# Optimization experiments

Measured on AMD Instinct MI355X. Metric: run time of the kernel, lower is better.

The kernel has to match this reference:

```python
import jax, jax.numpy as jnp
import numpy as np

N = 20000        # total nodes
E = 240000       # directed edges (avg in-degree 12); self-loops appended in reference
G = 50           # graphs in the batch
NPG = N // G     # nodes per graph
TD = 768         # text embedding dim
HC = 64          # hidden_channels
H = 8            # attention heads for conv1..conv3 (conv4 uses 1 head)
FD = 3 * HC * H + HC  # JK cat dim for num_layers=4
NEG = 0.2        # GATv2 leaky_relu negative slope
EPS = 1e-5       # GraphNorm eps


def setup_inputs() -> dict:
    key = jax.random.key(0)
    ks = iter(jax.random.split(key, 64))

    def w(shape, s=0.05):
        return jax.random.normal(next(ks), shape, dtype=jnp.float32) * s

    z = lambda *s: jnp.zeros(s, jnp.float32)
    o = lambda *s: jnp.ones(s, jnp.float32)

    inp = {
        'x': w((N, TD), 1.0),
        'edge_index': jax.random.randint(next(ks), (2, E), 0, N, dtype=jnp.int32),
        'batch': jnp.arange(N, dtype=jnp.int32) // NPG,
        'ptr': jnp.arange(G + 1, dtype=jnp.int32) * NPG,
        'tp_w': w((TD, HC)), 'tp_b': z(HC),
        'lin_w': w((FD, 1), 0.005), 'lin_b': z(1),
    }
    # GATv2Conv params: lin_l (source), lin_r (target), att, output bias
    for name, ind, heads, concat in [('c1', HC, H, True), ('c2', HC * H, H, True),
                                     ('c3', HC * H, H, True), ('c4', HC * H, 1, False)]:
        inp[name + '_wl'] = w((ind, heads * HC)); inp[name + '_bl'] = z(heads * HC)
        inp[name + '_wr'] = w((ind, heads * HC)); inp[name + '_br'] = z(heads * HC)
        inp[name + '_att'] = w((heads, HC))
        inp[name + '_bias'] = z(heads * HC if concat else HC)
    # GraphNorm params: weight, bias, mean_scale
    for name, d in [('n1', HC * H), ('n2', HC * H), ('n3', HC * H), ('n4', HC)]:
        inp[name + '_w'] = o(d); inp[name + '_b'] = z(d); inp[name + '_ms'] = o(d)
    return inp


def _gatv2(x, src, dst, wl, bl, wr, br, att, bias, heads, concat):
    # GATv2: e_ij = att . leaky_relu(W_l x_j + W_r x_i); alpha = softmax over in-neighbors of i
    xl = (x @ wl + bl).reshape(N, heads, HC)
    xr = (x @ wr + br).reshape(N, heads, HC)
    e = jax.nn.leaky_relu(xl[src] + xr[dst], NEG)           # [E', H, C]
    logit = jnp.einsum('ehc,hc->eh', e, att)                # [E', H]
    m = jax.ops.segment_max(logit, dst, num_segments=N)     # stable scatter-softmax
    p = jnp.exp(logit - m[dst])
    alpha = p / jax.ops.segment_sum(p, dst, num_segments=N)[dst]
    out = jax.ops.segment_sum(xl[src] * alpha[..., None], dst, num_segments=N)
    out = out.reshape(N, heads * HC) if concat else out.mean(axis=1)
    return out + bias


def _gnorm(x, batch, w, b, ms):
    # PyG GraphNorm: per-graph mean (scaled by mean_scale), per-graph std
    cnt = jax.ops.segment_sum(jnp.ones((N,), x.dtype), batch, num_segments=G)[:, None]
    mean = jax.ops.segment_sum(x, batch, num_segments=G) / cnt
    cen = x - ms * mean[batch]
    var = jax.ops.segment_sum(cen * cen, batch, num_segments=G) / cnt
    return w * cen / jnp.sqrt(var + EPS)[batch] + b


def reference(x, tp_w, tp_b,
              c1_wl, c1_bl, c1_wr, c1_br, c1_att, c1_bias,
              c2_wl, c2_bl, c2_wr, c2_br, c2_att, c2_bias,
              c3_wl, c3_bl, c3_wr, c3_br, c3_att, c3_bias,
              c4_wl, c4_bl, c4_wr, c4_br, c4_att, c4_bias,
              n1_w, n1_b, n1_ms, n2_w, n2_b, n2_ms,
              n3_w, n3_b, n3_ms, n4_w, n4_b, n4_ms,
              lin_w, lin_b, edge_index, batch, ptr):
    sl = jnp.arange(N, dtype=edge_index.dtype)
    src = jnp.concatenate([edge_index[0], sl])  # add_self_loops=True
    dst = jnp.concatenate([edge_index[1], sl])

    h = x @ tp_w + tp_b                          # text_proj (dropout = identity in eval)
    h = _gatv2(h, src, dst, c1_wl, c1_bl, c1_wr, c1_br, c1_att, c1_bias, H, True)
    h = jax.nn.elu(_gnorm(h, batch, n1_w, n1_b, n1_ms))
    xs = [h]
    h2 = _gatv2(h, src, dst, c2_wl, c2_bl, c2_wr, c2_br, c2_att, c2_bias, H, True)
    h = jax.nn.elu(_gnorm(h2 + h, batch, n2_w, n2_b, n2_ms))
    xs.append(h)
    h3 = _gatv2(h, src, dst, c3_wl, c3_bl, c3_wr, c3_br, c3_att, c3_bias, H, True)
    h = jax.nn.elu(_gnorm(h3 + h, batch, n3_w, n3_b, n3_ms))
    xs.append(h)
    h = _gnorm(_gatv2(h, src, dst, c4_wl, c4_bl, c4_wr, c4_br, c4_att, c4_bias, 1, False),
               batch, n4_w, n4_b, n4_ms)
    xs.append(h)

    xcat = jnp.concatenate(xs, axis=1)           # JumpingKnowledge cat -> [N, FD]
    out = xcat[ptr[:-1]] @ lin_w + lin_b         # summary node per graph -> [G, 1]
    return out.squeeze(-1)                       # num_classes==2 -> squeeze
```

## Files before the change

### kernel.cpp

```cpp
#include <hip/hip_runtime.h>
#include <hip/hip_bf16.h>

#define NEG_SLOPE 0.2f
#define EPSI 1e-5f
#define THR 8.0f

typedef __attribute__((ext_vector_type(8))) short bf16x8;
typedef __attribute__((ext_vector_type(4))) float f32x4;
typedef __attribute__((ext_vector_type(2))) float f32x2;

__device__ __forceinline__ float wred_sum(float v){
#pragma unroll
  for (int o = 32; o > 0; o >>= 1) v += __shfl_xor(v, o);
  return v;
}

__device__ __forceinline__ unsigned short f2bf(float f){
  __hip_bfloat16 h = __float2bfloat16(f);
  return *reinterpret_cast<unsigned short*>(&h);
}
__device__ __forceinline__ float bf2f(unsigned short u){
  return __uint_as_float((unsigned int)u << 16);
}
__device__ __forceinline__ f32x2 bfpair(unsigned int u){
  f32x2 r;
  r.x = __uint_as_float(u << 16);
  r.y = __uint_as_float(u & 0xffff0000u);
  return r;
}
__device__ __forceinline__ f32x2 vmax2(f32x2 a, f32x2 b){
#if __has_builtin(__builtin_elementwise_max)
  return __builtin_elementwise_max(a, b);
#else
  f32x2 r; r.x = fmaxf(a.x, b.x); r.y = fmaxf(a.y, b.y); return r;
#endif
}

__device__ __forceinline__ void gload16(const void* g, void* l){
  __builtin_amdgcn_global_load_lds((const __attribute__((address_space(1))) unsigned int*)g,
                                   (__attribute__((address_space(3))) unsigned int*)l, 16, 0, 0);
}

__global__ __launch_bounds__(256) void k_count(const int* __restrict__ ei, int* __restrict__ deg,
                                               int E, int EP){
  int e = blockIdx.x * 256 + threadIdx.x;
  if (e >= EP) return;
  int d = (e < E) ? ei[E + e] : (e - E);
  atomicAdd(&deg[d], 1);
}

__global__ __launch_bounds__(256) void k_scan(int* __restrict__ deg, int* __restrict__ rowptr, int n){
  __shared__ int part[256];
  int t = threadIdx.x;
  int L = (n + 255) / 256;
  int lo = t * L, hi = min(lo + L, n);
  int s = 0;
  for (int i = lo; i < hi; i++) s += deg[i];
  part[t] = s;
  __syncthreads();
  if (t == 0){
    int acc = 0;
    for (int i = 0; i < 256; i++){ int v = part[i]; part[i] = acc; acc += v; }
  }
  __syncthreads();
  int acc = part[t];
  for (int i = lo; i < hi; i++){
    int d = deg[i];
    rowptr[i] = acc;
    deg[i] = acc;
    acc += d;
  }
  if (t == 255) rowptr[n] = acc;
}

__global__ __launch_bounds__(256) void k_fill(const int* __restrict__ ei, int* __restrict__ cursor,
                                              int* __restrict__ srcn, int E, int EP){
  int e = blockIdx.x * 256 + threadIdx.x;
  if (e >= EP) return;
  int s, d;
  if (e < E){ s = ei[e]; d = ei[E + e]; } else { s = d = e - E; }
  int pos = atomicAdd(&cursor[d], 1);
  srcn[pos] = s;
}

__global__ __launch_bounds__(256) void k_cvt_wt(const float* __restrict__ W,
                                                unsigned short* __restrict__ Wt,
                                                int K, int Ncol){
  __shared__ float t[32][33];
  int bx = blockIdx.x, by = blockIdx.y;
  int tx = threadIdx.x & 31, ty = threadIdx.x >> 5;
#pragma unroll
  for (int i = 0; i < 4; i++)
    t[ty + i * 8][tx] = W[(size_t)(by * 32 + ty + i * 8) * Ncol + bx * 32 + tx];
  __syncthreads();
#pragma unroll
  for (int i = 0; i < 4; i++)
    Wt[(size_t)(bx * 32 + ty + i * 8) * K + by * 32 + tx] = f2bf(t[tx][ty + i * 8]);
}

__global__ __launch_bounds__(256) void k_cvt_wt2(const float* __restrict__ Wa,
                                                 const float* __restrict__ Wb,
                                                 unsigned short* __restrict__ Wt,
                                                 int K, int Ncol){
  __shared__ float t[32][33];
  int half = gridDim.x >> 1;
  int isB = blockIdx.x >= half;
  const float* W = isB ? Wb : Wa;
  unsigned short* out = Wt + (isB ? (size_t)Ncol * K : 0);
  int bx = isB ? blockIdx.x - half : blockIdx.x;
  int by = blockIdx.y;
  int tx = threadIdx.x & 31, ty = threadIdx.x >> 5;
#pragma unroll
  for (int i = 0; i < 4; i++)
    t[ty + i * 8][tx] = W[(size_t)(by * 32 + ty + i * 8) * Ncol + bx * 32 + tx];
  __syncthreads();
#pragma unroll
  for (int i = 0; i < 4; i++)
    out[(size_t)(bx * 32 + ty + i * 8) * K + by * 32 + tx] = f2bf(t[tx][ty + i * 8]);
}

template<int BN>
__global__ __launch_bounds__(512) void k_gemm_mfma8(const unsigned short* __restrict__ A,
                                                    const unsigned short* __restrict__ Wt,
                                                    const float* __restrict__ ba,
                                                    const float* __restrict__ bb,
                                                    int bsplit,
                                                    unsigned short* __restrict__ Cb,
                                                    int M, int K, int Ncol){
  constexpr int NF = BN / 64;
  __shared__ unsigned short As[128 * 32];
  __shared__ unsigned short Bs[BN * 32];
  const int tid = threadIdx.x;
  const int w = tid >> 6, lane = tid & 63;
  const int wr = w >> 2, wc = w & 3;
  const int row0 = blockIdx.y * 128, col0 = blockIdx.x * BN;
  const int lr = lane & 15, lk = lane >> 4;
  const int swz = (lr >> 1) & 3;

  f32x4 acc[4][NF];
#pragma unroll
  for (int i = 0; i < 4; i++)
#pragma unroll
    for (int j = 0; j < NF; j++) acc[i][j] = (f32x4){0.f, 0.f, 0.f, 0.f};

  for (int k0 = 0; k0 < K; k0 += 32){
    for (int g0 = w * 64; g0 < 512; g0 += 512){
      int g = g0 + lane;
      int row = g >> 2, slot = g & 3;
      int kq = slot ^ ((row >> 1) & 3);
      int srow = row0 + row; if (srow >= M) srow = M - 1;
      gload16(&A[(size_t)srow * K + k0 + kq * 8], &As[(size_t)g0 * 8]);
    }
    for (int g0 = w * 64; g0 < BN * 4; g0 += 512){
      int g = g0 + lane;
      int col = g >> 2, slot = g & 3;
      int kq = slot ^ ((col >> 1) & 3);
      gload16(&Wt[(size_t)(col0 + col) * K + k0 + kq * 8], &Bs[(size_t)g0 * 8]);
    }
    __syncthreads();

    bf16x8 af[4], bf_[NF];
#pragma unroll
    for (int mi = 0; mi < 4; mi++){
      int rl = wr * 64 + mi * 16 + lr;
      af[mi] = *(const bf16x8*)&As[(rl * 4 + (lk ^ swz)) * 8];
    }
#pragma unroll
    for (int ni = 0; ni < NF; ni++){
      int cl = wc * (BN / 4) + ni * 16 + lr;
      bf_[ni] = *(const bf16x8*)&Bs[(cl * 4 + (lk ^ swz)) * 8];
    }
#pragma unroll
    for (int mi = 0; mi < 4; mi++)
#pragma unroll
      for (int ni = 0; ni < NF; ni++)
        acc[mi][ni] = __builtin_amdgcn_mfma_f32_16x16x32_bf16(af[mi], bf_[ni], acc[mi][ni], 0, 0, 0);
    __syncthreads();
  }

#pragma unroll
  for (int mi = 0; mi < 4; mi++){
#pragma unroll
    for (int ni = 0; ni < NF; ni++){
      int gc = col0 + wc * (BN / 4) + ni * 16 + lr;
      float bv = gc < bsplit ? ba[gc] : bb[gc - bsplit];
#pragma unroll
      for (int r = 0; r < 4; r++){
        int gr = row0 + wr * 64 + mi * 16 + lk * 4 + r;
        if (gr < M) Cb[(size_t)gr * Ncol + gc] = f2bf(acc[mi][ni][r] + bv);
      }
    }
  }
}

__global__ __launch_bounds__(512) void k_gemm_tp(const float* __restrict__ A,
                                                 const unsigned short* __restrict__ Wt,
                                                 const float* __restrict__ bias,
                                                 unsigned short* __restrict__ Cb,
                                                 int M, int K){
  __shared__ unsigned short As[128 * 32];
  __shared__ unsigned short Bs[64 * 32];
  const int tid = threadIdx.x;
  const int w = tid >> 6, lane = tid & 63;
  const int wr = w >> 2, wc = w & 3;
  const int row0 = blockIdx.y * 128;
  const int lr = lane & 15, lk = lane >> 4;
  const int swz = (lr >> 1) & 3;

  f32x4 acc[4];
#pragma unroll
  for (int i = 0; i < 4; i++) acc[i] = (f32x4){0.f, 0.f, 0.f, 0.f};

  for (int k0 = 0; k0 < K; k0 += 32){
    {
      int g = tid;
      int row = g >> 2, slot = g & 3;
      int kq = slot ^ ((row >> 1) & 3);
      int srow = row0 + row; if (srow >= M) srow = M - 1;
      const float* ap = &A[(size_t)srow * K + k0 + kq * 8];
      float4 f0 = *(const float4*)ap;
      float4 f1 = *(const float4*)(ap + 4);
      bf16x8 v;
      v[0] = (short)f2bf(f0.x); v[1] = (short)f2bf(f0.y);
      v[2] = (short)f2bf(f0.z); v[3] = (short)f2bf(f0.w);
      v[4] = (short)f2bf(f1.x); v[5] = (short)f2bf(f1.y);
      v[6] = (short)f2bf(f1.z); v[7] = (short)f2bf(f1.w);
      *(bf16x8*)&As[(size_t)g * 8] = v;
    }
    for (int g0 = w * 64; g0 < 256; g0 += 512){
      int g = g0 + lane;
      int col = g >> 2, slot = g & 3;
      int kq = slot ^ ((col >> 1) & 3);
      gload16(&Wt[(size_t)col * K + k0 + kq * 8], &Bs[(size_t)g0 * 8]);
    }
    __syncthreads();

    bf16x8 af[4], bfr;
#pragma unroll
    for (int mi = 0; mi < 4; mi++){
      int rl = wr * 64 + mi * 16 + lr;
      af[mi] = *(const bf16x8*)&As[(rl * 4 + (lk ^ swz)) * 8];
    }
    {
      int cl = wc * 16 + lr;
      bfr = *(const bf16x8*)&Bs[(cl * 4 + (lk ^ swz)) * 8];
    }
#pragma unroll
    for (int mi = 0; mi < 4; mi++)
      acc[mi] = __builtin_amdgcn_mfma_f32_16x16x32_bf16(af[mi], bfr, acc[mi], 0, 0, 0);
    __syncthreads();
  }

  int gc = wc * 16 + lr;
  float bv = bias[gc];
#pragma unroll
  for (int mi = 0; mi < 4; mi++)
#pragma unroll
    for (int r = 0; r < 4; r++){
      int gr = row0 + wr * 64 + mi * 16 + lk * 4 + r;
      if (gr < M) Cb[(size_t)gr * 64 + gc] = f2bf(acc[mi][r] + bv);
    }
}

__global__ __launch_bounds__(256) void k_gat_fused8(const unsigned short* __restrict__ xlrb,
                                                    const float* __restrict__ att,
                                                    const int* __restrict__ rowptr,
                                                    const int* __restrict__ srcn,
                                                    const float* __restrict__ bias,
                                                    const unsigned short* __restrict__ resb,
                                                    unsigned short* __restrict__ yb,
                                                    int N){
  __shared__ float lm[4][64], ls[4][64], lacc[4][64][9];
  const int tid = threadIdx.x;
  const int w = tid >> 6, lane = tid & 63;
  const int node = blockIdx.x * 2 + (w >> 1);
  const int half = w & 1;
  const int nc = min(node, N - 1);

  f32x2 xr2[4], av2[4];
  {
    uint4 ur = *(const uint4*)&xlrb[(size_t)nc * 1024 + 512 + lane * 8];
    xr2[0] = bfpair(ur.x); xr2[1] = bfpair(ur.y); xr2[2] = bfpair(ur.z); xr2[3] = bfpair(ur.w);
    float4 a0 = *(const float4*)&att[lane * 8];
    float4 a1 = *(const float4*)&att[lane * 8 + 4];
    av2[0] = (f32x2){a0.x, a0.y}; av2[1] = (f32x2){a0.z, a0.w};
    av2[2] = (f32x2){a1.x, a1.y}; av2[3] = (f32x2){a1.z, a1.w};
  }
  int e0 = rowptr[nc], e1 = rowptr[nc + 1];
  if (node >= N){ e0 = 0; e1 = 0; }
  int len = e1 - e0;
  int mid = e0 + ((len + 1) >> 1);
  int rs = half ? mid : e0;
  int re = half ? e1 : mid;

  float m0 = -1e30f, s0 = 0.f, m1 = -1e30f, s1 = 0.f;
  f32x2 acc0[4] = {}, acc1[4] = {};

  for (int base = rs; base < re; base += 64){
    int cnt = min(64, re - base);
    int sn = 0;
    if (lane < cnt) sn = srcn[base + lane];
    int k = 0;
    for (; k + 1 < cnt; k += 2){
      int ska = __shfl(sn, k);
      int skb = __shfl(sn, k + 1);
      uint4 ua = *(const uint4*)&xlrb[(size_t)ska * 1024 + lane * 8];
      uint4 ub = *(const uint4*)&xlrb[(size_t)skb * 1024 + lane * 8];
      f32x2 va[4], vb[4];
      va[0] = bfpair(ua.x); va[1] = bfpair(ua.y); va[2] = bfpair(ua.z); va[3] = bfpair(ua.w);
      vb[0] = bfpair(ub.x); vb[1] = bfpair(ub.y); vb[2] = bfpair(ub.z); vb[3] = bfpair(ub.w);
      f32x2 da = (f32x2){0.f, 0.f}, db = (f32x2){0.f, 0.f};
#pragma unroll
      for (int j = 0; j < 4; j++){
        f32x2 ta = va[j] + xr2[j];
        f32x2 tb = vb[j] + xr2[j];
        ta = vmax2(ta, ta * NEG_SLOPE);
        tb = vmax2(tb, tb * NEG_SLOPE);
        da += ta * av2[j];
        db += tb * av2[j];
      }
      float suma = da.x + da.y, sumb = db.x + db.y;
      suma += __shfl_xor(suma, 1); sumb += __shfl_xor(sumb, 1);
      suma += __shfl_xor(suma, 2); sumb += __shfl_xor(sumb, 2);
      suma += __shfl_xor(suma, 4); sumb += __shfl_xor(sumb, 4);
      if (__builtin_expect(__any(suma > m0 + THR), 0)){
        float mn = fmaxf(m0, suma);
        float cs = __expf(m0 - mn);
        float p  = __expf(suma - mn);
        s0 = s0 * cs + p;
#pragma unroll
        for (int j = 0; j < 4; j++) acc0[j] = acc0[j] * cs + va[j] * p;
        m0 = mn;
      } else {
        float p = __expf(suma - m0);
        s0 += p;
#pragma unroll
        for (int j = 0; j < 4; j++) acc0[j] += va[j] * p;
      }
      if (__builtin_expect(__any(sumb > m1 + THR), 0)){
        float mn = fmaxf(m1, sumb);
        float cs = __expf(m1 - mn);
        float p  = __expf(sumb - mn);
        s1 = s1 * cs + p;
#pragma unroll
        for (int j = 0; j < 4; j++) acc1[j] = acc1[j] * cs + vb[j] * p;
        m1 = mn;
      } else {
        float p = __expf(sumb - m1);
        s1 += p;
#pragma unroll
        for (int j = 0; j < 4; j++) acc1[j] += vb[j] * p;
      }
    }
    if (k < cnt){
      int ska = __shfl(sn, k);
      uint4 ua = *(const uint4*)&xlrb[(size_t)ska * 1024 + lane * 8];
      f32x2 va[4];
      va[0] = bfpair(ua.x); va[1] = bfpair(ua.y); va[2] = bfpair(ua.z); va[3] = bfpair(ua.w);
      f32x2 da = (f32x2){0.f, 0.f};
#pragma unroll
      for (int j = 0; j < 4; j++){
        f32x2 ta = va[j] + xr2[j];
        ta = vmax2(ta, ta * NEG_SLOPE);
        da += ta * av2[j];
      }
      float suma = da.x + da.y;
      suma += __shfl_xor(suma, 1);
      suma += __shfl_xor(suma, 2);
      suma += __shfl_xor(suma, 4);
      if (__builtin_expect(__any(suma > m0 + THR), 0)){
        float mn = fmaxf(m0, suma);
        float cs = __expf(m0 - mn);
        float p  = __expf(suma - mn);
        s0 = s0 * cs + p;
#pragma unroll
        for (int j = 0; j < 4; j++) acc0[j] = acc0[j] * cs + va[j] * p;
        m0 = mn;
      } else {
        float p = __expf(suma - m0);
        s0 += p;
#pragma unroll
        for (int j = 0; j < 4; j++) acc0[j] += va[j] * p;
      }
    }
  }

  float mW = fmaxf(m0, m1);
  float ca = __expf(m0 - mW), cb = __expf(m1 - mW);
  float sW = s0 * ca + s1 * cb;
  f32x2 aW[4];
#pragma unroll
  for (int j = 0; j < 4; j++) aW[j] = acc0[j] * ca + acc1[j] * cb;

  lm[w][lane] = mW; ls[w][lane] = sW;
#pragma unroll
  for (int j = 0; j < 4; j++){
    lacc[w][lane][2 * j]     = aW[j].x;
    lacc[w][lane][2 * j + 1] = aW[j].y;
  }
  __syncthreads();
  if (half || node >= N) return;

  float mo = lm[w + 1][lane], so = ls[w + 1][lane];
  float mm = fmaxf(mW, mo);
  float c0x = __expf(mW - mm), c1x = __expf(mo - mm);
  float s = sW * c0x + so * c1x;
  float inv = 1.f / s;

  float4 b0 = *(const float4*)&bias[lane * 8];
  float4 b1 = *(const float4*)&bias[lane * 8 + 4];
  f32x2 bi2[4] = {(f32x2){b0.x, b0.y}, (f32x2){b0.z, b0.w},
                  (f32x2){b1.x, b1.y}, (f32x2){b1.z, b1.w}};
  f32x2 re2[4] = {};
  size_t o = (size_t)node * 512 + lane * 8;
  if (resb){
    uint4 rr = *(const uint4*)&resb[o];
    re2[0] = bfpair(rr.x); re2[1] = bfpair(rr.y); re2[2] = bfpair(rr.z); re2[3] = bfpair(rr.w);
  }
  bf16x8 ov;
#pragma unroll
  for (int j = 0; j < 4; j++){
    f32x2 ao = (f32x2){lacc[w + 1][lane][2 * j], lacc[w + 1][lane][2 * j + 1]};
    f32x2 r = (aW[j] * c0x + ao * c1x) * inv + bi2[j] + re2[j];
    ov[2 * j]     = (short)f2bf(r.x);
    ov[2 * j + 1] = (short)f2bf(r.y);
  }
  *(bf16x8*)&yb[o] = ov;
}

__global__ __launch_bounds__(256) void k_gat_fused1(const unsigned short* __restrict__ xlr,
                                                    const float* __restrict__ att,
                                                    const int* __restrict__ rowptr,
                                                    const int* __restrict__ srcn,
                                                    const float* __restrict__ bias,
                                                    unsigned short* __restrict__ yb4,
                                                    int N){
  int node = (blockIdx.x * 256 + threadIdx.x) >> 6;
  int lane = threadIdx.x & 63;
  if (node >= N) return;
  float xrv = bf2f(xlr[(size_t)node * 128 + 64 + lane]);
  float attv = att[lane];
  int e0 = rowptr[node], e1 = rowptr[node + 1];
  float m = -1e30f, s = 0.f, acc = 0.f;
  for (int base = e0; base < e1; base += 64){
    int cnt = min(64, e1 - base);
    int sn = 0;
    if (lane < cnt) sn = srcn[base + lane];
    for (int k = 0; k < cnt; k++){
      int sk = __shfl(sn, k);
      float v = bf2f(xlr[(size_t)sk * 128 + lane]);
      float t = v + xrv;
      t = fmaxf(t, t * NEG_SLOPE);
      float sum = wred_sum(t * attv);
      if (sum > m + THR){
        float mn = fmaxf(m, sum);
        float cs = __expf(m - mn);
        float p  = __expf(sum - mn);
        s = s * cs + p;
        acc = acc * cs + p * v;
        m = mn;
      } else {
        float p = __expf(sum - m);
        s += p;
        acc += p * v;
      }
    }
  }
  yb4[(size_t)node * 64 + lane] = f2bf(acc / s + bias[lane]);
}

#define NCHUNK 16
__global__ __launch_bounds__(256) void k_gnorm_stats(const unsigned short* __restrict__ y,
                                                     const int* __restrict__ ptrg,
                                                     float* __restrict__ psum,
                                                     float* __restrict__ psq,
                                                     int OD){
  int g = blockIdx.x, chunk = blockIdx.z;
  int lane = threadIdx.x & 63, sub = threadIdx.x >> 6;
  int c = blockIdx.y * 64 + lane;
  int lo = ptrg[g], hi = ptrg[g + 1], len = hi - lo;
  int c0 = lo + (len * chunk) / NCHUNK, c1 = lo + (len * (chunk + 1)) / NCHUNK;
  float s = 0.f, q = 0.f;
  for (int i = c0 + sub; i < c1; i += 4){
    float v = bf2f(y[(size_t)i * OD + c]);
    s += v; q += v * v;
  }
  __shared__ float sm[4][64], sq2[4][64];
  sm[sub][lane] = s; sq2[sub][lane] = q;
  __syncthreads();
  if (sub == 0){
    s = sm[0][lane] + sm[1][lane] + sm[2][lane] + sm[3][lane];
    q = sq2[0][lane] + sq2[1][lane] + sq2[2][lane] + sq2[3][lane];
    size_t o = (size_t)(g * NCHUNK + chunk) * OD + c;
    psum[o] = s; psq[o] = q;
  }
}

__global__ __launch_bounds__(256) void k_gnorm_coef(const float* __restrict__ psum,
                                                    const float* __restrict__ psq,
                                                    const float* __restrict__ w,
                                                    const float* __restrict__ b,
                                                    const float* __restrict__ ms,
                                                    const int* __restrict__ ptrg,
                                                    float* __restrict__ cA,
                                                    float* __restrict__ cC,
                                                    int OD){
  int g = blockIdx.x;
  int len = ptrg[g + 1] - ptrg[g];
  float inv_n = 1.f / (float)len;
  for (int c = threadIdx.x; c < OD; c += 256){
    float s = 0.f, q = 0.f;
    for (int k = 0; k < NCHUNK; k++){
      size_t o = (size_t)(g * NCHUNK + k) * OD + c;
      s += psum[o]; q += psq[o];
    }
    float mean = s * inv_n, ey2 = q * inv_n;
    float m = ms[c];
    float var = ey2 - mean * mean * (2.f * m - m * m);
    float inv = rsqrtf(var + EPSI);
    float A = w[c] * inv;
    cA[(size_t)g * OD + c] = A;
    cC[(size_t)g * OD + c] = b[c] - A * m * mean;
  }
}

__global__ __launch_bounds__(256) void k_gnorm_apply(const unsigned short* __restrict__ y,
                                                     const int* __restrict__ batch,
                                                     const float* __restrict__ cA,
                                                     const float* __restrict__ cC,
                                                     unsigned short* __restrict__ outb,
                                                     const int* __restrict__ ptrg,
                                                     float* __restrict__ cat,
                                                     int catoff, int FD,
                                                     int OD, int total4, int do_elu){
  int idx = blockIdx.x * 256 + threadIdx.x;
  if (idx >= total4) return;
  int od4 = OD >> 2;
  int node = idx / od4;
  int c = (idx - node * od4) << 2;
  int g = batch[node];
  ushort4 uv = ((const ushort4*)y)[idx];
  float4 v = make_float4(bf2f(uv.x), bf2f(uv.y), bf2f(uv.z), bf2f(uv.w));
  float4 A = *(const float4*)&cA[(size_t)g * OD + c];
  float4 Cc = *(const float4*)&cC[(size_t)g * OD + c];
  float4 r;
  r.x = A.x * v.x + Cc.x;
  r.y = A.y * v.y + Cc.y;
  r.z = A.z * v.z + Cc.z;
  r.w = A.w * v.w + Cc.w;
  if (do_elu){
    r.x = r.x > 0.f ? r.x : expf(r.x) - 1.f;
    r.y = r.y > 0.f ? r.y : expf(r.y) - 1.f;
    r.z = r.z > 0.f ? r.z : expf(r.z) - 1.f;
    r.w = r.w > 0.f ? r.w : expf(r.w) - 1.f;
  }
  ushort4 ob;
  ob.x = f2bf(r.x); ob.y = f2bf(r.y); ob.z = f2bf(r.z); ob.w = f2bf(r.w);
  ((ushort4*)outb)[idx] = ob;
  if (node == ptrg[g])
    *(float4*)&cat[(size_t)g * FD + catoff + c] = r;
}

__global__ __launch_bounds__(256) void k_final(const float* __restrict__ cat,
                                               const float* __restrict__ lin_w,
                                               const float* __restrict__ lin_b,
                                               float* __restrict__ out, int FD){
  int g = blockIdx.x;
  float s = 0.f;
  for (int c = threadIdx.x; c < FD; c += 256) s += cat[(size_t)g * FD + c] * lin_w[c];
  s = wred_sum(s);
  __shared__ float sm[4];
  if ((threadIdx.x & 63) == 0) sm[threadIdx.x >> 6] = s;
  __syncthreads();
  if (threadIdx.x == 0) out[g] = sm[0] + sm[1] + sm[2] + sm[3] + lin_b[0];
}

extern "C" void kernel_launch(void* const* d_in, const int* in_sizes, int n_in,
                              void* d_out, int out_size, void* d_ws, size_t ws_size,
                              hipStream_t stream) {
  const int TD = 768, HC = 64, H = 8;
  const float* x     = (const float*)d_in[0];
  const int*   ei    = (const int*)d_in[1];
  const int*   batch = (const int*)d_in[2];
  const int*   ptrg  = (const int*)d_in[3];
  const float* tp_w  = (const float*)d_in[4];
  const float* tp_b  = (const float*)d_in[5];
  const float* lin_w = (const float*)d_in[6];
  const float* lin_b = (const float*)d_in[7];
  const float* cw[4][6];
  for (int l = 0; l < 4; l++)
    for (int j = 0; j < 6; j++) cw[l][j] = (const float*)d_in[8 + 6 * l + j];
  const float* nw[4][3];
  for (int l = 0; l < 4; l++)
    for (int j = 0; j < 3; j++) nw[l][j] = (const float*)d_in[32 + 3 * l + j];

  const int N  = in_sizes[0] / TD;
  const int E  = in_sizes[1] / 2;
  const int EP = E + N;
  const int G  = in_sizes[3] - 1;
  const int FD = 3 * HC * H + HC;

  char* wsp = (char*)d_ws;
  size_t off = 0;
  auto alloc = [&](size_t b) -> void* {
    void* p = wsp + off;
    off += (b + 255) & ~(size_t)255;
    return p;
  };
  unsigned short* xlrb = (unsigned short*)alloc((size_t)N * 1024 * 2);
  unsigned short* yb   = (unsigned short*)alloc((size_t)N * 512 * 2);
  unsigned short* actA = (unsigned short*)alloc((size_t)N * 512 * 2);
  unsigned short* h0h  = (unsigned short*)alloc((size_t)N * 64 * 2);
  int*   rowptr= (int*)alloc((size_t)(N + 1) * 4);
  int*   cursor= (int*)alloc((size_t)N * 4);
  int*   srcn  = (int*)alloc((size_t)EP * 4);
  float* cat   = (float*)alloc((size_t)G * FD * 4);
  float* psum  = (float*)alloc((size_t)G * NCHUNK * 512 * 4);
  float* psq   = (float*)alloc((size_t)G * NCHUNK * 512 * 4);
  float* cA    = (float*)alloc((size_t)G * 512 * 4);
  float* cC    = (float*)alloc((size_t)G * 512 * 4);
  unsigned short* WtLR = (unsigned short*)alloc((size_t)1024 * 512 * 2);
  unsigned short* WtTP = (unsigned short*)alloc((size_t)64 * 768 * 2);
  unsigned short* Wt4  = (unsigned short*)alloc((size_t)128 * 512 * 2);
  (void)ws_size; (void)n_in; (void)out_size;

  float* out = (float*)d_out;

  unsigned short* xlr4b = xlrb;
  unsigned short* yb4   = yb;

  hipMemsetAsync(cursor, 0, (size_t)N * 4, stream);
  int eblk = (EP + 255) / 256;
  k_count<<<eblk, 256, 0, stream>>>(ei, cursor, E, EP);
  k_scan<<<1, 256, 0, stream>>>(cursor, rowptr, N);
  k_fill<<<eblk, 256, 0, stream>>>(ei, cursor, srcn, E, EP);

  const int mfmaRows = (N + 127) / 128;
  const int nb8 = (N + 1) / 2;
  const int nodeBlocks = (N + 3) / 4;

  k_cvt_wt<<<dim3(2, TD / 32), 256, 0, stream>>>(tp_w, WtTP, TD, 64);
  k_gemm_tp<<<dim3(1, mfmaRows), 512, 0, stream>>>(x, WtTP, tp_b, h0h, N, TD);

  auto layer8 = [&](const unsigned short* actbf, int Kin, int l,
                    const unsigned short* resb, int catoff){
    k_cvt_wt2<<<dim3(32, Kin / 32), 256, 0, stream>>>(cw[l][0], cw[l][2], WtLR, Kin, 512);
    k_gemm_mfma8<256><<<dim3(4, mfmaRows), 512, 0, stream>>>(actbf, WtLR, cw[l][1], cw[l][3], 512,
                                                             xlrb, N, Kin, 1024);
    k_gat_fused8<<<nb8, 256, 0, stream>>>(xlrb, cw[l][4], rowptr, srcn,
                                          cw[l][5], resb, yb, N);
    k_gnorm_stats<<<dim3(G, 8, NCHUNK), 256, 0, stream>>>(yb, ptrg, psum, psq, 512);
    k_gnorm_coef<<<G, 256, 0, stream>>>(psum, psq, nw[l][0], nw[l][1], nw[l][2], ptrg, cA, cC, 512);
    int total4 = N * 128;
    k_gnorm_apply<<<(total4 + 255) / 256, 256, 0, stream>>>(yb, batch, cA, cC, actA,
                                                            ptrg, cat, catoff, FD,
                                                            512, total4, 1);
  };

  layer8(h0h,  64,  0, nullptr, 0);
  layer8(actA, 512, 1, actA,    512);
  layer8(actA, 512, 2, actA,    1024);

  k_cvt_wt2<<<dim3(4, 16), 256, 0, stream>>>(cw[3][0], cw[3][2], Wt4, 512, 64);
  k_gemm_mfma8<128><<<dim3(1, mfmaRows), 512, 0, stream>>>(actA, Wt4, cw[3][1], cw[3][3], 64,
                                                           xlr4b, N, 512, 128);
  k_gat_fused1<<<nodeBlocks, 256, 0, stream>>>(xlr4b, cw[3][4], rowptr, srcn,
                                               cw[3][5], yb4, N);
  k_gnorm_stats<<<dim3(G, 1, NCHUNK), 256, 0, stream>>>(yb4, ptrg, psum, psq, 64);
  k_gnorm_coef<<<G, 256, 0, stream>>>(psum, psq, nw[3][0], nw[3][1], nw[3][2], ptrg, cA, cC, 64);
  k_gnorm_apply<<<(N * 16 + 255) / 256, 256, 0, stream>>>(yb4, batch, cA, cC, h0h,
                                                          ptrg, cat, 1536, FD,
                                                          64, N * 16, 0);

  k_final<<<G, 256, 0, stream>>>(cat, lin_w, lin_b, out, FD);
}
```

Measured before the change: 509.7 us.

## Add BK=64 MFMA GEMM, use one wave per node in GAT, split softmax chains

Adds a new GEMM kernel with a 64-wide K tile and an XOR-swizzled shared-memory layout, used for the 8-head layer projections, which halves the number of K-loop iterations and barriers. The 8-head GAT aggregation now gives each node a single wave instead of splitting its edges across two waves, which removes the shared-memory merge and the block barrier. The 1-head GAT kernel processes edges with four independent online-softmax accumulators to expose more instruction-level parallelism. In exchange, the GEMM uses more LDS per block, and the GAT kernel has less parallelism for high-degree nodes.

After: 491.1 us. 1.04x faster.

```diff
diff --git a/kernel.cpp b/kernel.cpp
--- a/kernel.cpp
+++ b/kernel.cpp
@@ -117,6 +117,84 @@
 #pragma unroll
   for (int i = 0; i < 4; i++)
     out[(size_t)(bx * 32 + ty + i * 8) * K + by * 32 + tx] = f2bf(t[tx][ty + i * 8]);
+}
+
+__global__ __launch_bounds__(512) void k_gemm_b64(const unsigned short* __restrict__ A,
+                                                  const unsigned short* __restrict__ Wt,
+                                                  const float* __restrict__ ba,
+                                                  const float* __restrict__ bb,
+                                                  int bsplit,
+                                                  unsigned short* __restrict__ Cb,
+                                                  int M, int K, int Ncol){
+  __shared__ unsigned short As[128 * 64];
+  __shared__ unsigned short Bs[256 * 64];
+  const int tid = threadIdx.x;
+  const int w = tid >> 6, lane = tid & 63;
+  const int wr = w >> 2, wc = w & 3;
+  const int row0 = blockIdx.y * 128, col0 = blockIdx.x * 256;
+  const int lr = lane & 15, lk = lane >> 4;
+
+  f32x4 acc[4][4];
+#pragma unroll
+  for (int i = 0; i < 4; i++)
+#pragma unroll
+    for (int j = 0; j < 4; j++) acc[i][j] = (f32x4){0.f, 0.f, 0.f, 0.f};
+
+  for (int k0 = 0; k0 < K; k0 += 64){
+#pragma unroll
+    for (int t = 0; t < 2; t++){
+      int g = w * 64 + lane + t * 512;
+      int row = g >> 3, slot = g & 7;
+      int kq = slot ^ ((row >> 1) & 7);
+      int srow = row0 + row; if (srow >= M) srow = M - 1;
+      gload16(&A[(size_t)srow * K + k0 + kq * 8], &As[(size_t)(w * 64 + t * 512) * 8]);
+    }
+#pragma unroll
+    for (int t = 0; t < 4; t++){
+      int g = w * 64 + lane + t * 512;
+      int col = g >> 3, slot = g & 7;
+      int kq = slot ^ ((col >> 1) & 7);
+      gload16(&Wt[(size_t)(col0 + col) * K + k0 + kq * 8], &Bs[(size_t)(w * 64 + t * 512) * 8]);
+    }
+    __syncthreads();
+
+#pragma unroll
+    for (int ph = 0; ph < 2; ph++){
+      bf16x8 af[4], bf_[4];
+#pragma unroll
+      for (int mi = 0; mi < 4; mi++){
+        int rl = wr * 64 + mi * 16 + lr;
+        int sl = (ph * 4 + lk) ^ ((rl >> 1) & 7);
+        af[mi] = *(const bf16x8*)&As[(rl * 8 + sl) * 8];
+      }
+#pragma unroll
+      for (int ni = 0; ni < 4; ni++){
+        int cl = wc * 64 + ni * 16 + lr;
+        int sl = (ph * 4 + lk) ^ ((cl >> 1) & 7);
+        bf_[ni] = *(const bf16x8*)&Bs[(cl * 8 + sl) * 8];
+      }
+#pragma unroll
+      for (int mi = 0; mi < 4; mi++)
+#pragma unroll
+        for (int ni = 0; ni < 4; ni++)
+          acc[mi][ni] = __builtin_amdgcn_mfma_f32_16x16x32_bf16(af[mi], bf_[ni], acc[mi][ni], 0, 0, 0);
+    }
+    __syncthreads();
+  }
+
+#pragma unroll
+  for (int mi = 0; mi < 4; mi++){
+#pragma unroll
+    for (int ni = 0; ni < 4; ni++){
+      int gc = col0 + wc * 64 + ni * 16 + lr;
+      float bv = gc < bsplit ? ba[gc] : bb[gc - bsplit];
+#pragma unroll
+      for (int r = 0; r < 4; r++){
+        int gr = row0 + wr * 64 + mi * 16 + lk * 4 + r;
+        if (gr < M) Cb[(size_t)gr * Ncol + gc] = f2bf(acc[mi][ni][r] + bv);
+      }
+    }
+  }
 }
 
 template<int BN>
@@ -270,34 +348,24 @@
                                                     const unsigned short* __restrict__ resb,
                                                     unsigned short* __restrict__ yb,
                                                     int N){
-  __shared__ float lm[4][64], ls[4][64], lacc[4][64][9];
-  const int tid = threadIdx.x;
-  const int w = tid >> 6, lane = tid & 63;
-  const int node = blockIdx.x * 2 + (w >> 1);
-  const int half = w & 1;
-  const int nc = min(node, N - 1);
-
+  int node = (blockIdx.x * 256 + threadIdx.x) >> 6;
+  int lane = threadIdx.x & 63;
+  if (node >= N) return;
   f32x2 xr2[4], av2[4];
   {
-    uint4 ur = *(const uint4*)&xlrb[(size_t)nc * 1024 + 512 + lane * 8];
+    uint4 ur = *(const uint4*)&xlrb[(size_t)node * 1024 + 512 + lane * 8];
     xr2[0] = bfpair(ur.x); xr2[1] = bfpair(ur.y); xr2[2] = bfpair(ur.z); xr2[3] = bfpair(ur.w);
     float4 a0 = *(const float4*)&att[lane * 8];
     float4 a1 = *(const float4*)&att[lane * 8 + 4];
     av2[0] = (f32x2){a0.x, a0.y}; av2[1] = (f32x2){a0.z, a0.w};
     av2[2] = (f32x2){a1.x, a1.y}; av2[3] = (f32x2){a1.z, a1.w};
   }
-  int e0 = rowptr[nc], e1 = rowptr[nc + 1];
-  if (node >= N){ e0 = 0; e1 = 0; }
-  int len = e1 - e0;
-  int mid = e0 + ((len + 1) >> 1);
-  int rs = half ? mid : e0;
-  int re = half ? e1 : mid;
-
+  int e0 = rowptr[node], e1 = rowptr[node + 1];
   float m0 = -1e30f, s0 = 0.f, m1 = -1e30f, s1 = 0.f;
   f32x2 acc0[4] = {}, acc1[4] = {};
 
-  for (int base = rs; base < re; base += 64){
-    int cnt = min(64, re - base);
+  for (int base = e0; base < e1; base += 64){
+    int cnt = min(64, e1 - base);
     int sn = 0;
     if (lane < cnt) sn = srcn[base + lane];
     int k = 0;
@@ -384,29 +452,10 @@
       }
     }
   }
-
-  float mW = fmaxf(m0, m1);
-  float ca = __expf(m0 - mW), cb = __expf(m1 - mW);
-  float sW = s0 * ca + s1 * cb;
-  f32x2 aW[4];
-#pragma unroll
-  for (int j = 0; j < 4; j++) aW[j] = acc0[j] * ca + acc1[j] * cb;
-
-  lm[w][lane] = mW; ls[w][lane] = sW;
-#pragma unroll
-  for (int j = 0; j < 4; j++){
-    lacc[w][lane][2 * j]     = aW[j].x;
-    lacc[w][lane][2 * j + 1] = aW[j].y;
-  }
-  __syncthreads();
-  if (half || node >= N) return;
-
-  float mo = lm[w + 1][lane], so = ls[w + 1][lane];
-  float mm = fmaxf(mW, mo);
-  float c0x = __expf(mW - mm), c1x = __expf(mo - mm);
-  float s = sW * c0x + so * c1x;
+  float m = fmaxf(m0, m1);
+  float c0 = __expf(m0 - m), c1 = __expf(m1 - m);
+  float s = s0 * c0 + s1 * c1;
   float inv = 1.f / s;
-
   float4 b0 = *(const float4*)&bias[lane * 8];
   float4 b1 = *(const float4*)&bias[lane * 8 + 4];
   f32x2 bi2[4] = {(f32x2){b0.x, b0.y}, (f32x2){b0.z, b0.w},
@@ -420,8 +469,7 @@
   bf16x8 ov;
 #pragma unroll
   for (int j = 0; j < 4; j++){
-    f32x2 ao = (f32x2){lacc[w + 1][lane][2 * j], lacc[w + 1][lane][2 * j + 1]};
-    f32x2 r = (aW[j] * c0x + ao * c1x) * inv + bi2[j] + re2[j];
+    f32x2 r = (acc0[j] * c0 + acc1[j] * c1) * inv + bi2[j] + re2[j];
     ov[2 * j]     = (short)f2bf(r.x);
     ov[2 * j + 1] = (short)f2bf(r.y);
   }
@@ -441,32 +489,47 @@
   float xrv = bf2f(xlr[(size_t)node * 128 + 64 + lane]);
   float attv = att[lane];
   int e0 = rowptr[node], e1 = rowptr[node + 1];
-  float m = -1e30f, s = 0.f, acc = 0.f;
+  float m[4] = {-1e30f, -1e30f, -1e30f, -1e30f};
+  float s[4] = {0.f, 0.f, 0.f, 0.f};
+  float acc[4] = {0.f, 0.f, 0.f, 0.f};
   for (int base = e0; base < e1; base += 64){
     int cnt = min(64, e1 - base);
     int sn = 0;
     if (lane < cnt) sn = srcn[base + lane];
-    for (int k = 0; k < cnt; k++){
-      int sk = __shfl(sn, k);
-      float v = bf2f(xlr[(size_t)sk * 128 + lane]);
-      float t = v + xrv;
-      t = fmaxf(t, t * NEG_SLOPE);
-      float sum = wred_sum(t * attv);
-      if (sum > m + THR){
-        float mn = fmaxf(m, sum);
-        float cs = __expf(m - mn);
-        float p  = __expf(sum - mn);
-        s = s * cs + p;
-        acc = acc * cs + p * v;
-        m = mn;
-      } else {
-        float p = __expf(sum - m);
-        s += p;
-        acc += p * v;
-      }
-    }
-  }
-  yb4[(size_t)node * 64 + lane] = f2bf(acc / s + bias[lane]);
+    for (int k = 0; k < cnt; k += 4){
+#pragma unroll
+      for (int j = 0; j < 4; j++){
+        if (k + j < cnt){
+          int sk = __shfl(sn, k + j);
+          float v = bf2f(xlr[(size_t)sk * 128 + lane]);
+          float t = v + xrv;
+          t = fmaxf(t, t * NEG_SLOPE);
+          float sum = wred_sum(t * attv);
+          if (sum > m[j] + THR){
+            float mn = fmaxf(m[j], sum);
+            float cs = __expf(m[j] - mn);
+            float p  = __expf(sum - mn);
+            s[j] = s[j] * cs + p;
+            acc[j] = acc[j] * cs + p * v;
+            m[j] = mn;
+          } else {
+            float p = __expf(sum - m[j]);
+            s[j] += p;
+            acc[j] += p * v;
+          }
+        }
+      }
+    }
+  }
+  float mm = fmaxf(fmaxf(m[0], m[1]), fmaxf(m[2], m[3]));
+  float st = 0.f, at = 0.f;
+#pragma unroll
+  for (int j = 0; j < 4; j++){
+    float c = __expf(m[j] - mm);
+    st += s[j] * c;
+    at += acc[j] * c;
+  }
+  yb4[(size_t)node * 64 + lane] = f2bf(at / st + bias[lane]);
 }
 
 #define NCHUNK 16
@@ -636,7 +699,6 @@
   k_fill<<<eblk, 256, 0, stream>>>(ei, cursor, srcn, E, EP);
 
   const int mfmaRows = (N + 127) / 128;
-  const int nb8 = (N + 1) / 2;
   const int nodeBlocks = (N + 3) / 4;
 
   k_cvt_wt<<<dim3(2, TD / 32), 256, 0, stream>>>(tp_w, WtTP, TD, 64);
@@ -645,10 +707,10 @@
   auto layer8 = [&](const unsigned short* actbf, int Kin, int l,
                     const unsigned short* resb, int catoff){
     k_cvt_wt2<<<dim3(32, Kin / 32), 256, 0, stream>>>(cw[l][0], cw[l][2], WtLR, Kin, 512);
-    k_gemm_mfma8<256><<<dim3(4, mfmaRows), 512, 0, stream>>>(actbf, WtLR, cw[l][1], cw[l][3], 512,
-                                                             xlrb, N, Kin, 1024);
-    k_gat_fused8<<<nb8, 256, 0, stream>>>(xlrb, cw[l][4], rowptr, srcn,
-                                          cw[l][5], resb, yb, N);
+    k_gemm_b64<<<dim3(4, mfmaRows), 512, 0, stream>>>(actbf, WtLR, cw[l][1], cw[l][3], 512,
+                                                      xlrb, N, Kin, 1024);
+    k_gat_fused8<<<nodeBlocks, 256, 0, stream>>>(xlrb, cw[l][4], rowptr, srcn,
+                                                 cw[l][5], resb, yb, N);
     k_gnorm_stats<<<dim3(G, 8, NCHUNK), 256, 0, stream>>>(yb, ptrg, psum, psq, 512);
     k_gnorm_coef<<<G, 256, 0, stream>>>(psum, psq, nw[l][0], nw[l][1], nw[l][2], ptrg, cA, cC, 512);
     int total4 = N * 128;
```
